# Optimization experiments

Measured on AMD Instinct MI355X. Metric: run time of the kernel, lower is better.

Reference implementation:

```python
import jax, jax.numpy as jnp
import numpy as np

HEADS = 8
DIM_HEAD = 64
SCALE = DIM_HEAD ** -0.5


def setup_inputs() -> dict:
    key = jax.random.key(0)
    k1, k2, k3 = jax.random.split(key, 3)
    B, C, L = 4, 512, 2048
    h_dim = HEADS * DIM_HEAD  # 512
    x = jax.random.normal(k1, (B, C, L), dtype=jnp.float32)
    w_qkv = jax.random.normal(k2, (C, 3 * h_dim), dtype=jnp.float32) * (C ** -0.5)
    w_out = jax.random.normal(k3, (h_dim, C), dtype=jnp.float32) * (h_dim ** -0.5)
    b_out = jnp.zeros((C,), dtype=jnp.float32)
    return {"x": x, "w_qkv": w_qkv, "w_out": w_out, "b_out": b_out}


def reference(x, w_qkv, w_out, b_out):
    B, C, L = x.shape
    # pointwise conv (kernel size 1, no bias): [B,C,L] x [C,3hd] -> [B,3hd,L]
    qkv = jnp.einsum('bcl,cf->bfl', x, w_qkv)
    q, k, v = jnp.split(qkv, 3, axis=1)  # each [B, h*d, L]
    def to_heads(t):
        return t.reshape(B, HEADS, DIM_HEAD, L)  # b h d l
    q, k, v = to_heads(q), to_heads(k), to_heads(v)
    q = q * SCALE
    sim = jnp.einsum('bhdi,bhdj->bhij', q, k)  # [B,H,L,L]
    attn = jax.nn.softmax(sim, axis=-1)  # stable (max-subtract) softmax
    out = jnp.einsum('bhij,bhdj->bhid', attn, v)  # [B,H,L,D]
    # rearrange 'b h l c -> b (h c) l'
    out = out.transpose(0, 1, 3, 2).reshape(B, HEADS * DIM_HEAD, L)
    # to_out pointwise conv with bias: [B,hd,L] -> [B,C,L]
    return jnp.einsum('bcl,cf->bfl', out, w_out) + b_out[None, :, None]
```

## Files before the change

kernel.cpp:

```cpp
#include <hip/hip_runtime.h>


#define LDIM 2048
#define CDIM 512
#define BATCH 4

typedef __attribute__((ext_vector_type(8))) short s16x8;
typedef __attribute__((ext_vector_type(4))) float f32x4;
typedef __attribute__((ext_vector_type(4))) unsigned short u16x4;
typedef unsigned int u32;
typedef unsigned short u16;

__device__ __forceinline__ u16 f2b(float f) {
    unsigned u = __float_as_uint(f);
    u += 0x7fffu + ((u >> 16) & 1u);
    return (u16)(u >> 16);
}
__device__ __forceinline__ u32 pk2(float a, float b) {
    u32 ua = __float_as_uint(a) + 0x8000u;
    u32 ub = __float_as_uint(b) + 0x8000u;
    return __builtin_amdgcn_perm(ub, ua, 0x07060302u);
}

__global__ __launch_bounds__(256)
void transpA_k(const float* __restrict__ x, const float* __restrict__ wq,
               const float* __restrict__ wo, u16* __restrict__ XP,
               u16* __restrict__ WP, u16* __restrict__ WOP)
{
    const int r0 = blockIdx.x * 64;
    const int y  = blockIdx.y;
    const float* in; u16* out; int inLD, c0;
    if (y < 128) {
        const int b = y >> 5, ct = y & 31;
        in = x + (size_t)b * CDIM * LDIM; inLD = LDIM; c0 = ct * 64;
        out = XP + (size_t)b * LDIM * CDIM;
    } else if (y < 152) {
        in = wq; inLD = 1536; c0 = (y - 128) * 64; out = WP;
    } else {
        in = wo; inLD = 512;  c0 = (y - 152) * 64; out = WOP;
    }

    __shared__ __align__(16) u16 t[64][80];
    const int tt = threadIdx.x;
    const int lr = tt >> 4, lc = (tt & 15) * 4;
    #pragma unroll
    for (int i = 0; i < 4; ++i) {
        f32x4 v = *(const f32x4*)(in + (size_t)(r0 + lr + i * 16) * inLD + c0 + lc);
        #pragma unroll
        for (int j = 0; j < 4; ++j) t[lc + j][lr + i * 16] = f2b(v[j]);
    }
    __syncthreads();
    const int orow = tt >> 2, ocg = (tt & 3) * 16;
    s16x8 v0 = *(const s16x8*)&t[orow][ocg];
    s16x8 v1 = *(const s16x8*)&t[orow][ocg + 8];
    const int row   = c0 + orow;
    const int rtile = row >> 4, rr = row & 15;
    const int cstep = (r0 + ocg) >> 5;
    const int qb    = (ocg >> 3) & 3;
    u16* dst = out + ((size_t)(rtile * 16 + cstep) * 64 + qb * 16 + rr) * 8;
    *(s16x8*)dst = v0;
    *(s16x8*)(dst + 128) = v1;
}

__global__ __launch_bounds__(256)
void qkvgemm_bf16(const u16* __restrict__ XP, const u16* __restrict__ WP,
                  u16* __restrict__ QF, u16* __restrict__ KF, u16* __restrict__ VF)
{
    const int f0 = blockIdx.x * 64;
    const int l0 = blockIdx.y * 128;
    const int b  = blockIdx.z;
    const u16* xTb = XP + (size_t)b * LDIM * CDIM;
    const int t = threadIdx.x, w = t >> 6, lane = t & 63;
    const int mn = lane & 15, q = lane >> 4;
    const bool vpart = (f0 >= 1024);

    const u16 *Abase, *Bbase;
    int mbase, nbase;
    if (!vpart) {
        mbase = f0 + (w >> 1) * 32; nbase = l0 + (w & 1) * 64;
        Abase = WP + (size_t)mbase * CDIM; Bbase = xTb + (size_t)nbase * CDIM;
    } else {
        mbase = l0 + w * 32; nbase = f0;
        Abase = xTb + (size_t)mbase * CDIM; Bbase = WP + (size_t)nbase * CDIM;
    }

    f32x4 acc[2][4] = {};
    #pragma unroll 2
    for (int c0 = 0; c0 < CDIM; c0 += 32) {
        s16x8 a[2], bf[4];
        #pragma unroll
        for (int mi = 0; mi < 2; ++mi)
            a[mi] = *(const s16x8*)(Abase + mi * 16 * CDIM + c0 * 16 + lane * 8);
        #pragma unroll
        for (int ni = 0; ni < 4; ++ni)
            bf[ni] = *(const s16x8*)(Bbase + ni * 16 * CDIM + c0 * 16 + lane * 8);
        #pragma unroll
        for (int mi = 0; mi < 2; ++mi)
            #pragma unroll
            for (int ni = 0; ni < 4; ++ni)
                acc[mi][ni] = __builtin_amdgcn_mfma_f32_16x16x32_bf16(a[mi], bf[ni], acc[mi][ni], 0, 0, 0);
    }

    if (!vpart) {
        const int part = f0 >> 9;
        const float sc2 = (part == 0) ? 0.18033688f : 1.0f;
        u16* Tout = (part == 0) ? QF : KF;
        #pragma unroll
        for (int mi = 0; mi < 2; ++mi) {
            const int fg0 = mbase + mi * 16;
            const int h = (fg0 >> 6) & 7;
            const int d0 = (fg0 & 63) + q * 4;
            const int kd = d0 >> 5, qq = (d0 >> 3) & 3, e0 = d0 & 7;
            u16* T = Tout + (size_t)(b * 8 + h) * LDIM * 64;
            #pragma unroll
            for (int ni = 0; ni < 4; ++ni) {
                const int lg = nbase + ni * 16 + mn;
                size_t addr;
                if (part == 0) {
                    const int i32 = lg >> 5, ibt = (lg >> 4) & 1, mnq = lg & 15;
                    addr = (size_t)(((i32 * 2 + ibt) * 2 + kd) * 512 + (qq * 16 + mnq) * 8 + e0);
                } else {
                    const int j64 = lg >> 6, r6 = lg & 63;
                    const int jt  = ((r6 >> 2) & 1) * 2 + (r6 >> 5);
                    const int mnk = ((r6 >> 3) & 3) * 4 + (r6 & 3);
                    addr = (size_t)(((j64 * 4 + jt) * 2 + kd) * 512 + (qq * 16 + mnk) * 8 + e0);
                }
                u16x4 pk;
                #pragma unroll
                for (int r = 0; r < 4; ++r) pk[r] = f2b(acc[mi][ni][r] * sc2);
                *(u16x4*)(T + addr) = pk;
            }
        }
    } else {
        #pragma unroll
        for (int ni = 0; ni < 4; ++ni) {
            const int fg = nbase + ni * 16 + mn;
            const int h = (fg >> 6) & 7;
            const int d = fg & 63;
            const int dt = d >> 4, mnv = d & 15;
            u16* Vb = VF + (size_t)(b * 8 + h) * LDIM * 64;
            #pragma unroll
            for (int mi = 0; mi < 2; ++mi) {
                const int lg0 = mbase + mi * 16 + q * 4;
                const int j64 = lg0 >> 6, j6 = lg0 & 63;
                const int kj = j6 >> 5, qq = (j6 >> 3) & 3, e0 = j6 & 7;
                const size_t addr = (size_t)(((j64 * 2 + kj) * 4 + dt) * 512 + (qq * 16 + mnv) * 8 + e0);
                u16x4 pk;
                #pragma unroll
                for (int r = 0; r < 4; ++r) pk[r] = f2b(acc[mi][ni][r]);
                *(u16x4*)(Vb + addr) = pk;
            }
        }
    }
}

__global__ __launch_bounds__(128)
void attn_k(const u16* __restrict__ QF, const u16* __restrict__ KF,
            const u16* __restrict__ VF, u16* __restrict__ aoP)
{
    const int bh = blockIdx.x;
    const int b = bh >> 3, h = bh & 7;
    const u16* Qh = QF + (size_t)bh * LDIM * 64;
    const u16* Kh = KF + (size_t)bh * LDIM * 64;
    const u16* Vh = VF + (size_t)bh * LDIM * 64;

    __shared__ __align__(16) float o_sh[32][68];
    __shared__ float lp_sh[32];

    const int tid = threadIdx.x;
    const int wv = tid >> 6;
    const int lane = tid & 63;
    const int mn = lane & 15, q = lane >> 4;
    const int i32 = blockIdx.y;
    const int iw = i32 * 32;
    const int NT = LDIM / 64;
    const int TH = NT / 2;
    const int tbase = wv * TH;

    s16x8 aq[2][2];
    #pragma unroll
    for (int ibt = 0; ibt < 2; ++ibt)
        #pragma unroll
        for (int kd = 0; kd < 2; ++kd)
            aq[ibt][kd] = *(const s16x8*)(Qh + (size_t)(((i32 * 2 + ibt) * 2 + kd) * 512) + lane * 8);

    f32x4 o_acc[2][4] = {};
    float lp[2] = {0.f, 0.f};

    s16x8 kc[2][4], vc[2][4];
    {
        const u16* Kt = Kh + (size_t)tbase * 4096;
        const u16* Vt = Vh + (size_t)tbase * 4096;
        #pragma unroll
        for (int kd = 0; kd < 2; ++kd)
            #pragma unroll
            for (int jt = 0; jt < 4; ++jt)
                kc[kd][jt] = *(const s16x8*)(Kt + ((jt * 2 + kd) << 9) + (lane << 3));
        #pragma unroll
        for (int kj = 0; kj < 2; ++kj)
            #pragma unroll
            for (int dt = 0; dt < 4; ++dt)
                vc[kj][dt] = *(const s16x8*)(Vt + ((kj * 4 + dt) << 9) + (lane << 3));
    }

    #pragma unroll 2
    for (int jj = 0; jj < TH; ++jj) {
        const int tn = tbase + ((jj + 1) & (TH - 1));

        s16x8 kn[2][4], vn[2][4];
        {
            const u16* Kt = Kh + (size_t)tn * 4096;
            const u16* Vt = Vh + (size_t)tn * 4096;
            #pragma unroll
            for (int kd = 0; kd < 2; ++kd)
                #pragma unroll
                for (int jt = 0; jt < 4; ++jt)
                    kn[kd][jt] = *(const s16x8*)(Kt + ((jt * 2 + kd) << 9) + (lane << 3));
            #pragma unroll
            for (int kj = 0; kj < 2; ++kj)
                #pragma unroll
                for (int dt = 0; dt < 4; ++dt)
                    vn[kj][dt] = *(const s16x8*)(Vt + ((kj * 4 + dt) << 9) + (lane << 3));
        }

        f32x4 s[2][4] = {};
        #pragma unroll
        for (int kd = 0; kd < 2; ++kd)
            #pragma unroll
            for (int jt = 0; jt < 4; ++jt) {
                s[0][jt] = __builtin_amdgcn_mfma_f32_16x16x32_bf16(kc[kd][jt], aq[0][kd], s[0][jt], 0, 0, 0);
                s[1][jt] = __builtin_amdgcn_mfma_f32_16x16x32_bf16(kc[kd][jt], aq[1][kd], s[1][jt], 0, 0, 0);
            }

        #pragma unroll
        for (int kj = 0; kj < 2; ++kj) {
            s16x8 ap[2];
            #pragma unroll
            for (int ibt = 0; ibt < 2; ++ibt) {
                float pa0 = __builtin_amdgcn_exp2f(s[ibt][kj][0]);
                float pa1 = __builtin_amdgcn_exp2f(s[ibt][kj][1]);
                float pa2 = __builtin_amdgcn_exp2f(s[ibt][kj][2]);
                float pa3 = __builtin_amdgcn_exp2f(s[ibt][kj][3]);
                float pb0 = __builtin_amdgcn_exp2f(s[ibt][kj + 2][0]);
                float pb1 = __builtin_amdgcn_exp2f(s[ibt][kj + 2][1]);
                float pb2 = __builtin_amdgcn_exp2f(s[ibt][kj + 2][2]);
                float pb3 = __builtin_amdgcn_exp2f(s[ibt][kj + 2][3]);
                lp[ibt] += ((pa0 + pa1) + (pa2 + pa3)) + ((pb0 + pb1) + (pb2 + pb3));
                union { s16x8 v; u32 w[4]; } u;
                u.w[0] = pk2(pa0, pa1);
                u.w[1] = pk2(pa2, pa3);
                u.w[2] = pk2(pb0, pb1);
                u.w[3] = pk2(pb2, pb3);
                ap[ibt] = u.v;
            }
            #pragma unroll
            for (int dt = 0; dt < 4; ++dt) {
                o_acc[0][dt] = __builtin_amdgcn_mfma_f32_16x16x32_bf16(vc[kj][dt], ap[0], o_acc[0][dt], 0, 0, 0);
                o_acc[1][dt] = __builtin_amdgcn_mfma_f32_16x16x32_bf16(vc[kj][dt], ap[1], o_acc[1][dt], 0, 0, 0);
            }
        }

        #pragma unroll
        for (int kd = 0; kd < 2; ++kd)
            #pragma unroll
            for (int jt = 0; jt < 4; ++jt)
                kc[kd][jt] = kn[kd][jt];
        #pragma unroll
        for (int kj = 0; kj < 2; ++kj)
            #pragma unroll
            for (int dt = 0; dt < 4; ++dt)
                vc[kj][dt] = vn[kj][dt];
    }

    #pragma unroll
    for (int ibt = 0; ibt < 2; ++ibt) {
        lp[ibt] += __shfl_xor(lp[ibt], 16);
        lp[ibt] += __shfl_xor(lp[ibt], 32);
    }

    if (wv == 1) {
        #pragma unroll
        for (int ibt = 0; ibt < 2; ++ibt) {
            #pragma unroll
            for (int dt = 0; dt < 4; ++dt)
                *(f32x4*)&o_sh[ibt * 16 + mn][dt * 16 + q * 4] = o_acc[ibt][dt];
            if (q == 0) lp_sh[ibt * 16 + mn] = lp[ibt];
        }
    }
    __syncthreads();
    if (wv == 0) {
        u16* Ab = aoP + (size_t)b * LDIM * 512;
        #pragma unroll
        for (int ibt = 0; ibt < 2; ++ibt) {
            const float rinv = 1.0f / (lp[ibt] + lp_sh[ibt * 16 + mn]);
            const int ltile = (iw >> 4) + ibt;
            #pragma unroll
            for (int dt = 0; dt < 4; ++dt) {
                f32x4 os = *(const f32x4*)&o_sh[ibt * 16 + mn][dt * 16 + q * 4];
                u16x4 pk;
                #pragma unroll
                for (int r = 0; r < 4; ++r)
                    pk[r] = f2b((o_acc[ibt][dt][r] + os[r]) * rinv);
                const int cstep = h * 2 + (dt >> 1);
                const int lanep = ((dt & 1) * 2 + (q >> 1)) * 16 + mn;
                u16* dst = Ab + ((size_t)(ltile * 16 + cstep) * 64 + lanep) * 8 + (q & 1) * 4;
                *(u16x4*)dst = pk;
            }
        }
    }
}

__global__ __launch_bounds__(256)
void outgemm_d(const u16* __restrict__ aoP, const u16* __restrict__ WOP,
               const float* __restrict__ bias, float* __restrict__ Y)
{
    const int f0 = blockIdx.x * 64;
    const int l0 = blockIdx.y * 128;
    const int b  = blockIdx.z;
    const int t = threadIdx.x, w = t >> 6, lane = t & 63;
    const int mn = lane & 15, q = lane >> 4;
    const int mbase = f0 + (w >> 1) * 32;
    const int nbase = l0 + (w & 1) * 64;
    const u16* Abase = WOP + (size_t)mbase * CDIM;
    const u16* Bbase = aoP + ((size_t)b * LDIM + nbase) * CDIM;
    float* Yb = Y + (size_t)b * CDIM * LDIM;

    f32x4 acc[2][4] = {};
    #pragma unroll 2
    for (int c0 = 0; c0 < CDIM; c0 += 32) {
        s16x8 a[2], bf[4];
        #pragma unroll
        for (int mi = 0; mi < 2; ++mi)
            a[mi] = *(const s16x8*)(Abase + mi * 16 * CDIM + c0 * 16 + lane * 8);
        #pragma unroll
        for (int ni = 0; ni < 4; ++ni)
            bf[ni] = *(const s16x8*)(Bbase + ni * 16 * CDIM + c0 * 16 + lane * 8);
        #pragma unroll
        for (int mi = 0; mi < 2; ++mi)
            #pragma unroll
            for (int ni = 0; ni < 4; ++ni)
                acc[mi][ni] = __builtin_amdgcn_mfma_f32_16x16x32_bf16(a[mi], bf[ni], acc[mi][ni], 0, 0, 0);
    }
    #pragma unroll
    for (int mi = 0; mi < 2; ++mi)
        #pragma unroll
        for (int r = 0; r < 4; ++r) {
            const int f = mbase + mi * 16 + q * 4 + r;
            const float bs = bias[f];
            #pragma unroll
            for (int ni = 0; ni < 4; ++ni)
                Yb[(size_t)f * LDIM + nbase + ni * 16 + mn] = acc[mi][ni][r] + bs;
        }
}

extern "C" void kernel_launch(void* const* d_in, const int* in_sizes, int n_in,
                              void* d_out, int out_size, void* d_ws, size_t ws_size,
                              hipStream_t stream) {
    const float *x = nullptr, *w_qkv = nullptr, *w_out = nullptr, *b_out = nullptr;
    for (int i = 0; i < n_in; ++i) {
        switch (in_sizes[i]) {
            case 4 * 512 * 2048: x     = (const float*)d_in[i]; break;
            case 512 * 1536:     w_qkv = (const float*)d_in[i]; break;
            case 512 * 512:      w_out = (const float*)d_in[i]; break;
            case 512:            b_out = (const float*)d_in[i]; break;
        }
    }
    float* out = (float*)d_out;

    const size_t SLAB = (size_t)BATCH * LDIM * 512;
    u16* WOP = (u16*)d_ws;
    u16* XP  = WOP + (size_t)512 * 512;
    u16* WP  = XP + SLAB;
    u16* QF  = WP + (size_t)1536 * 512;
    u16* KF  = QF + SLAB;
    u16* VF  = KF + SLAB;
    u16* aoP = VF + SLAB;

    transpA_k<<<dim3(8, 160), 256, 0, stream>>>(x, w_qkv, w_out, XP, WP, WOP);
    qkvgemm_bf16<<<dim3(24, 16, BATCH), 256, 0, stream>>>(XP, WP, QF, KF, VF);
    attn_k<<<dim3(32, 64), 128, 0, stream>>>(QF, KF, VF, aoP);
    outgemm_d<<<dim3(8, 16, BATCH), 256, 0, stream>>>(aoP, WOP, b_out, out);
}
```

Measured before the change: 190.1 us.

## Process 64 query rows per attention block to halve K/V reloads

Each attention block now handles 64 query rows (four 16-row tiles) instead of 32, so every K/V tile loaded from global memory is reused across twice as many MFMA operations, and the grid shrinks to 1024 blocks. The V prefetch is moved after the QK^T MFMAs, which shortens register live ranges and overlaps the V load with compute. The Q store layout is simplified to a linear 16-row-tile index, consistent with the new indexing. In exchange, accumulators and score registers double, which raises register pressure and may lower occupancy, and there are fewer blocks to spread across CUs.

```diff
diff --git a/kernel.cpp b/kernel.cpp
--- a/kernel.cpp
+++ b/kernel.cpp
@@ -117,8 +117,8 @@
                 const int lg = nbase + ni * 16 + mn;
                 size_t addr;
                 if (part == 0) {
-                    const int i32 = lg >> 5, ibt = (lg >> 4) & 1, mnq = lg & 15;
-                    addr = (size_t)(((i32 * 2 + ibt) * 2 + kd) * 512 + (qq * 16 + mnq) * 8 + e0);
+                    const int t16 = lg >> 4, mnq = lg & 15;
+                    addr = (size_t)((t16 * 2 + kd) * 512 + (qq * 16 + mnq) * 8 + e0);
                 } else {
                     const int j64 = lg >> 6, r6 = lg & 63;
                     const int jt  = ((r6 >> 2) & 1) * 2 + (r6 >> 5);
@@ -164,28 +164,28 @@
     const u16* Kh = KF + (size_t)bh * LDIM * 64;
     const u16* Vh = VF + (size_t)bh * LDIM * 64;
 
-    __shared__ __align__(16) float o_sh[32][68];
-    __shared__ float lp_sh[32];
+    __shared__ __align__(16) float o_sh[64][68];
+    __shared__ float lp_sh[64];
 
     const int tid = threadIdx.x;
     const int wv = tid >> 6;
     const int lane = tid & 63;
     const int mn = lane & 15, q = lane >> 4;
-    const int i32 = blockIdx.y;
-    const int iw = i32 * 32;
-    const int NT = LDIM / 64;
-    const int TH = NT / 2;
+    const int ib64 = blockIdx.y;
+    const int TH = 16;
     const int tbase = wv * TH;
 
-    s16x8 aq[2][2];
+    s16x8 aq[4][2];
     #pragma unroll
-    for (int ibt = 0; ibt < 2; ++ibt)
-        #pragma unroll
-        for (int kd = 0; kd < 2; ++kd)
-            aq[ibt][kd] = *(const s16x8*)(Qh + (size_t)(((i32 * 2 + ibt) * 2 + kd) * 512) + lane * 8);
-
-    f32x4 o_acc[2][4] = {};
-    float lp[2] = {0.f, 0.f};
+    for (int ibt = 0; ibt < 4; ++ibt) {
+        const int t16 = ib64 * 4 + ibt;
+        #pragma unroll
+        for (int kd = 0; kd < 2; ++kd)
+            aq[ibt][kd] = *(const s16x8*)(Qh + (size_t)((t16 * 2 + kd) * 512) + lane * 8);
+    }
+
+    f32x4 o_acc[4][4] = {};
+    float lp[4] = {0.f, 0.f, 0.f, 0.f};
 
     s16x8 kc[2][4], vc[2][4];
     {
@@ -206,37 +206,37 @@
     #pragma unroll 2
     for (int jj = 0; jj < TH; ++jj) {
         const int tn = tbase + ((jj + 1) & (TH - 1));
-
-        s16x8 kn[2][4], vn[2][4];
-        {
-            const u16* Kt = Kh + (size_t)tn * 4096;
-            const u16* Vt = Vh + (size_t)tn * 4096;
-            #pragma unroll
-            for (int kd = 0; kd < 2; ++kd)
-                #pragma unroll
-                for (int jt = 0; jt < 4; ++jt)
-                    kn[kd][jt] = *(const s16x8*)(Kt + ((jt * 2 + kd) << 9) + (lane << 3));
-            #pragma unroll
-            for (int kj = 0; kj < 2; ++kj)
-                #pragma unroll
-                for (int dt = 0; dt < 4; ++dt)
-                    vn[kj][dt] = *(const s16x8*)(Vt + ((kj * 4 + dt) << 9) + (lane << 3));
-        }
-
-        f32x4 s[2][4] = {};
-        #pragma unroll
-        for (int kd = 0; kd < 2; ++kd)
-            #pragma unroll
-            for (int jt = 0; jt < 4; ++jt) {
-                s[0][jt] = __builtin_amdgcn_mfma_f32_16x16x32_bf16(kc[kd][jt], aq[0][kd], s[0][jt], 0, 0, 0);
-                s[1][jt] = __builtin_amdgcn_mfma_f32_16x16x32_bf16(kc[kd][jt], aq[1][kd], s[1][jt], 0, 0, 0);
-            }
+        const u16* Kt = Kh + (size_t)tn * 4096;
+        const u16* Vt = Vh + (size_t)tn * 4096;
+
+        s16x8 kn[2][4];
+        #pragma unroll
+        for (int kd = 0; kd < 2; ++kd)
+            #pragma unroll
+            for (int jt = 0; jt < 4; ++jt)
+                kn[kd][jt] = *(const s16x8*)(Kt + ((jt * 2 + kd) << 9) + (lane << 3));
+
+        f32x4 s[4][4] = {};
+        #pragma unroll
+        for (int kd = 0; kd < 2; ++kd)
+            #pragma unroll
+            for (int jt = 0; jt < 4; ++jt)
+                #pragma unroll
+                for (int ibt = 0; ibt < 4; ++ibt)
+                    s[ibt][jt] = __builtin_amdgcn_mfma_f32_16x16x32_bf16(kc[kd][jt], aq[ibt][kd], s[ibt][jt], 0, 0, 0);
+
+        s16x8 vn[2][4];
+        #pragma unroll
+        for (int kj = 0; kj < 2; ++kj)
+            #pragma unroll
+            for (int dt = 0; dt < 4; ++dt)
+                vn[kj][dt] = *(const s16x8*)(Vt + ((kj * 4 + dt) << 9) + (lane << 3));
 
         #pragma unroll
         for (int kj = 0; kj < 2; ++kj) {
-            s16x8 ap[2];
-            #pragma unroll
-            for (int ibt = 0; ibt < 2; ++ibt) {
+            s16x8 ap[4];
+            #pragma unroll
+            for (int ibt = 0; ibt < 4; ++ibt) {
                 float pa0 = __builtin_amdgcn_exp2f(s[ibt][kj][0]);
                 float pa1 = __builtin_amdgcn_exp2f(s[ibt][kj][1]);
                 float pa2 = __builtin_amdgcn_exp2f(s[ibt][kj][2]);
@@ -254,10 +254,10 @@
                 ap[ibt] = u.v;
             }
             #pragma unroll
-            for (int dt = 0; dt < 4; ++dt) {
-                o_acc[0][dt] = __builtin_amdgcn_mfma_f32_16x16x32_bf16(vc[kj][dt], ap[0], o_acc[0][dt], 0, 0, 0);
-                o_acc[1][dt] = __builtin_amdgcn_mfma_f32_16x16x32_bf16(vc[kj][dt], ap[1], o_acc[1][dt], 0, 0, 0);
-            }
+            for (int dt = 0; dt < 4; ++dt)
+                #pragma unroll
+                for (int ibt = 0; ibt < 4; ++ibt)
+                    o_acc[ibt][dt] = __builtin_amdgcn_mfma_f32_16x16x32_bf16(vc[kj][dt], ap[ibt], o_acc[ibt][dt], 0, 0, 0);
         }
 
         #pragma unroll
@@ -273,14 +273,14 @@
     }
 
     #pragma unroll
-    for (int ibt = 0; ibt < 2; ++ibt) {
+    for (int ibt = 0; ibt < 4; ++ibt) {
         lp[ibt] += __shfl_xor(lp[ibt], 16);
         lp[ibt] += __shfl_xor(lp[ibt], 32);
     }
 
     if (wv == 1) {
         #pragma unroll
-        for (int ibt = 0; ibt < 2; ++ibt) {
+        for (int ibt = 0; ibt < 4; ++ibt) {
             #pragma unroll
             for (int dt = 0; dt < 4; ++dt)
                 *(f32x4*)&o_sh[ibt * 16 + mn][dt * 16 + q * 4] = o_acc[ibt][dt];
@@ -291,9 +291,9 @@
     if (wv == 0) {
         u16* Ab = aoP + (size_t)b * LDIM * 512;
         #pragma unroll
-        for (int ibt = 0; ibt < 2; ++ibt) {
+        for (int ibt = 0; ibt < 4; ++ibt) {
             const float rinv = 1.0f / (lp[ibt] + lp_sh[ibt * 16 + mn]);
-            const int ltile = (iw >> 4) + ibt;
+            const int ltile = ib64 * 4 + ibt;
             #pragma unroll
             for (int dt = 0; dt < 4; ++dt) {
                 f32x4 os = *(const f32x4*)&o_sh[ibt * 16 + mn][dt * 16 + q * 4];
@@ -378,6 +378,6 @@
 
     transpA_k<<<dim3(8, 160), 256, 0, stream>>>(x, w_qkv, w_out, XP, WP, WOP);
     qkvgemm_bf16<<<dim3(24, 16, BATCH), 256, 0, stream>>>(XP, WP, QF, KF, VF);
-    attn_k<<<dim3(32, 64), 128, 0, stream>>>(QF, KF, VF, aoP);
+    attn_k<<<dim3(32, 32), 128, 0, stream>>>(QF, KF, VF, aoP);
     outgemm_d<<<dim3(8, 16, BATCH), 256, 0, stream>>>(aoP, WOP, b_out, out);
 }
```

Result: faster. 176.7 us (-7.1%).
